# Optimization experiments

Measured on AMD Instinct MI355X. Metric: run time of the kernel, lower is better.

Reference implementation:

```python
import jax, jax.numpy as jnp
import numpy as np

N = 50000      # nodes
E = 800000     # edges (before self loops)
F_IN = 128     # dataset.num_features
HID = 32       # hidden_channels (per GAT head)
HEADS = 4
C = 40         # dataset.num_classes
NEG_SLOPE = 0.2


def setup_inputs() -> dict:
    key = jax.random.key(0)
    ks = jax.random.split(key, 18)
    g = lambda k, shape, fan: jax.random.normal(k, shape, dtype=jnp.float32) / np.sqrt(fan)
    inp = {
        "x": jax.random.normal(ks[0], (N, F_IN), dtype=jnp.float32),
        "edge_index": jax.random.randint(ks[1], (2, E), 0, N, dtype=jnp.int64),
        # GAT layer 1: F_IN -> HEADS*HID
        "gat_W1": g(ks[2], (F_IN, HEADS * HID), F_IN),
        "gat_att_src1": g(ks[3], (HEADS, HID), HID),
        "gat_att_dst1": g(ks[4], (HEADS, HID), HID),
        "gat_b1": jnp.zeros((HEADS * HID,), jnp.float32),
        # GAT layer 2: HEADS*HID -> C, heads=1
        "gat_W2": g(ks[5], (HEADS * HID, C), HEADS * HID),
        "gat_att_src2": g(ks[6], (1, C), C),
        "gat_att_dst2": g(ks[7], (1, C), C),
        "gat_b2": jnp.zeros((C,), jnp.float32),
        # GCN layers
        "gcn_W1": g(ks[8], (F_IN, HID), F_IN),
        "gcn_b1": jnp.zeros((HID,), jnp.float32),
        "gcn_W2": g(ks[9], (HID, C), HID),
        "gcn_b2": jnp.zeros((C,), jnp.float32),
        # final linear: 2C -> C
        "lin_W": g(ks[10], (2 * C, C), 2 * C),
        "lin_b": jnp.zeros((C,), jnp.float32),
        "weight_c": jnp.float32(0.5),
        "weight_t": jnp.float32(0.5),
    }
    return inp


def _add_self_loops(src, dst, n):
    loop = jnp.arange(n, dtype=src.dtype)
    return jnp.concatenate([src, loop]), jnp.concatenate([dst, loop])


def _gat_conv(x, src, dst, n, W, att_src, att_dst, b, heads, out_dim):
    # h: [n, heads, out_dim]
    h = (x @ W).reshape(n, heads, out_dim)
    a_s = jnp.einsum('nhd,hd->nh', h, att_src)   # source-side attention logit
    a_d = jnp.einsum('nhd,hd->nh', h, att_dst)   # target-side attention logit
    e = jax.nn.leaky_relu(a_s[src] + a_d[dst], NEG_SLOPE)  # [E', heads]
    # softmax over incoming edges of each target node (self loops guarantee >=1 edge)
    m = jax.ops.segment_max(e, dst, num_segments=n)
    ex = jnp.exp(e - m[dst])
    s = jax.ops.segment_sum(ex, dst, num_segments=n)
    alpha = ex / s[dst]                          # [E', heads]
    out = jax.ops.segment_sum(h[src] * alpha[..., None], dst, num_segments=n)
    return out.reshape(n, heads * out_dim) + b


def _gcn_conv(x, src, dst, n, W, b):
    h = x @ W
    deg = jax.ops.segment_sum(jnp.ones(src.shape, h.dtype), dst, num_segments=n)
    norm = jax.lax.rsqrt(deg)                    # deg >= 1 (self loops)
    coef = (norm[src] * norm[dst])[:, None]
    return jax.ops.segment_sum(h[src] * coef, dst, num_segments=n) + b


def reference(x, edge_index, gat_W1, gat_att_src1, gat_att_dst1, gat_b1,
              gat_W2, gat_att_src2, gat_att_dst2, gat_b2,
              gcn_W1, gcn_b1, gcn_W2, gcn_b2, lin_W, lin_b,
              weight_c, weight_t):
    n = x.shape[0]
    src, dst = _add_self_loops(edge_index[0], edge_index[1], n)
    # GAT branch (dropout is identity at inference)
    x_gat = _gat_conv(x, src, dst, n, gat_W1, gat_att_src1, gat_att_dst1,
                      gat_b1, HEADS, HID)
    x_gat = jax.nn.elu(x_gat)
    x_gat = _gat_conv(x_gat, src, dst, n, gat_W2, gat_att_src2, gat_att_dst2,
                      gat_b2, 1, C)
    # GCN branch
    x_gcn = jax.nn.relu(_gcn_conv(x, src, dst, n, gcn_W1, gcn_b1))
    x_gcn = _gcn_conv(x_gcn, src, dst, n, gcn_W2, gcn_b2)
    # weighted feature concat + linear head
    cat = jnp.concatenate([x_gcn * weight_c, x_gat * weight_t], axis=1)  # [n, 2C]
    return cat @ lin_W + lin_b
```

## Files before the change

### kernel.cpp

```cpp
#include <hip/hip_runtime.h>
#include <math.h>

#define F_IN   128
#define HIDC   32
#define NHEAD  4
#define CDIM   40
#define NEG_SLOPE 0.2f
#define BCAP   4096
#define OVCAP  16384
#define SCHUNK 4096

typedef __attribute__((ext_vector_type(8))) short bf16x8;
typedef __attribute__((ext_vector_type(4))) float f32x4;

__device__ __forceinline__ float leakyf(float x) { return x > 0.f ? x : NEG_SLOPE * x; }

__device__ __forceinline__ float wred_sum(float v) {
#pragma unroll
    for (int o = 32; o > 0; o >>= 1) v += __shfl_xor(v, o, 64);
    return v;
}
__device__ __forceinline__ float sel4(float4 v, int h) {
    return (h == 0) ? v.x : (h == 1) ? v.y : (h == 2) ? v.z : v.w;
}
__device__ __forceinline__ unsigned pack2_bf16(float a, float b) {
    unsigned ua = __float_as_uint(a);
    unsigned ub = __float_as_uint(b);
    ua = (ua + 0x7FFFu + ((ua >> 16) & 1u)) >> 16;
    ub = (ub + 0x7FFFu + ((ub >> 16) & 1u)) >> 16;
    return ua | (ub << 16);
}
__device__ __forceinline__ float2 unpack2_bf16(unsigned p) {
    return make_float2(__uint_as_float(p << 16), __uint_as_float(p & 0xFFFF0000u));
}
__device__ __forceinline__ float bf2f(unsigned short u) {
    return __uint_as_float(((unsigned)u) << 16);
}

__global__ void wb_prep_kernel(const float* __restrict__ Wg, const float* __restrict__ Wc,
                               uint4* __restrict__ wbf)
{
    int b = blockIdx.x;
    int lane = threadIdx.x;
    int nt = b >> 2, ks = b & 3;
    int c = nt * 16 + (lane & 15);
    int k0 = ks * 32 + (lane >> 4) * 8;
    unsigned u[4];
#pragma unroll
    for (int jj = 0; jj < 4; ++jj) {
        int k = k0 + 2 * jj;
        float a0 = (c < 128) ? Wg[(size_t)k * 128 + c] : Wc[(size_t)k * 32 + (c - 128)];
        float a1 = (c < 128) ? Wg[(size_t)(k + 1) * 128 + c] : Wc[(size_t)(k + 1) * 32 + (c - 128)];
        u[jj] = pack2_bf16(a0, a1);
    }
    wbf[(size_t)b * 64 + lane] = make_uint4(u[0], u[1], u[2], u[3]);
}

__global__ __launch_bounds__(256) void gemm1_mfma_kernel(
    const float* __restrict__ X, const uint4* __restrict__ wbf,
    const float* __restrict__ aw_s, const float* __restrict__ aw_d,
    unsigned* __restrict__ h1b, unsigned* __restrict__ g1b,
    float* __restrict__ as1, float* __restrict__ ad1, int n)
{
    __shared__ float Ct[64][164];
    __shared__ float sw[128], dw[128];
    const int tid = threadIdx.x;
    const int w = tid >> 6, lane = tid & 63;
    const int m = lane & 15, q = lane >> 4;
    const int node0 = blockIdx.x * 64;
    if (tid < 128) { sw[tid] = aw_s[tid]; dw[tid] = aw_d[tid]; }

    f32x4 acc[10];
#pragma unroll
    for (int t = 0; t < 10; ++t) acc[t] = (f32x4){0.f, 0.f, 0.f, 0.f};

    const int row = node0 + w * 16 + m;
    const bool rv = row < n;
#pragma unroll
    for (int ks = 0; ks < 4; ++ks) {
        uint4 pa = make_uint4(0u, 0u, 0u, 0u);
        if (rv) {
            const float* xr = X + (size_t)row * 128 + ks * 32 + q * 8;
            float4 a0 = *(const float4*)xr;
            float4 a1 = *(const float4*)(xr + 4);
            pa = make_uint4(pack2_bf16(a0.x, a0.y), pack2_bf16(a0.z, a0.w),
                            pack2_bf16(a1.x, a1.y), pack2_bf16(a1.z, a1.w));
        }
        bf16x8 af = *(bf16x8*)&pa;
#pragma unroll
        for (int nt = 0; nt < 10; ++nt) {
            uint4 pb = wbf[(size_t)(nt * 4 + ks) * 64 + lane];
            bf16x8 bfv = *(bf16x8*)&pb;
            acc[nt] = __builtin_amdgcn_mfma_f32_16x16x32_bf16(af, bfv, acc[nt], 0, 0, 0);
        }
    }
#pragma unroll
    for (int nt = 0; nt < 10; ++nt)
#pragma unroll
        for (int r = 0; r < 4; ++r)
            Ct[w * 16 + q * 4 + r][nt * 16 + m] = acc[nt][r];
    __syncthreads();

    for (int i = tid; i < 64 * 64; i += 256) {
        int nd = i >> 6, u = i & 63;
        int gn = node0 + nd;
        if (gn < n)
            h1b[(size_t)gn * 64 + u] = pack2_bf16(Ct[nd][2 * u], Ct[nd][2 * u + 1]);
    }
    for (int i = tid; i < 64 * 16; i += 256) {
        int nd = i >> 4, u = i & 15;
        int gn = node0 + nd;
        if (gn < n)
            g1b[(size_t)gn * 16 + u] = pack2_bf16(Ct[nd][128 + 2 * u], Ct[nd][128 + 2 * u + 1]);
    }
    {
        int nd = tid >> 2, h = tid & 3;
        int gn = node0 + nd;
        if (gn < n) {
            float s = 0.f, d = 0.f;
#pragma unroll
            for (int k = 0; k < HIDC; ++k) {
                float v = Ct[nd][h * HIDC + k];
                s = fmaf(v, sw[h * HIDC + k], s);
                d = fmaf(v, dw[h * HIDC + k], d);
            }
            as1[(size_t)gn * 4 + h] = s;
            ad1[(size_t)gn * 4 + h] = d;
        }
    }
}

template<int K, int OUTC, int BN, int BK, int OSTRIDE = OUTC>
__global__ __launch_bounds__((OUTC / 4) * (BN / 4)) void gemm_tile(
    const float* __restrict__ X, const float* __restrict__ W,
    const float* __restrict__ bias, float* __restrict__ Y, int n)
{
    constexpr int CG = OUTC / 4;
    constexpr int NG = BN / 4;
    constexpr int NT = CG * NG;
    __shared__ float Xs[BK][BN + 4];
    __shared__ float Ws[BK][OUTC];
    const int tid = threadIdx.x;
    const int cg = tid % CG, ng = tid / CG;
    const int node0 = blockIdx.x * BN;
    float acc[4][4] = {};

    for (int kb = 0; kb < K; kb += BK) {
        for (int idx = tid; idx < BN * (BK / 4); idx += NT) {
            int nd = idx / (BK / 4);
            int kq = idx % (BK / 4);
            int gnode = node0 + nd;
            float4 v = (gnode < n) ? *(const float4*)&X[(size_t)gnode * K + kb + kq * 4]
                                   : make_float4(0.f, 0.f, 0.f, 0.f);
            Xs[kq * 4 + 0][nd] = v.x;
            Xs[kq * 4 + 1][nd] = v.y;
            Xs[kq * 4 + 2][nd] = v.z;
            Xs[kq * 4 + 3][nd] = v.w;
        }
        for (int idx = tid; idx < BK * CG; idx += NT) {
            int kk = idx / CG;
            int cq = idx % CG;
            *(float4*)&Ws[kk][cq * 4] = *(const float4*)&W[(size_t)(kb + kk) * OUTC + cq * 4];
        }
        __syncthreads();
#pragma unroll
        for (int k = 0; k < BK; ++k) {
            float4 xv = *(const float4*)&Xs[k][ng * 4];
            float4 wv = *(const float4*)&Ws[k][cg * 4];
            float xa[4] = {xv.x, xv.y, xv.z, xv.w};
            float wa[4] = {wv.x, wv.y, wv.z, wv.w};
#pragma unroll
            for (int j = 0; j < 4; ++j)
#pragma unroll
                for (int c = 0; c < 4; ++c)
                    acc[j][c] = fmaf(xa[j], wa[c], acc[j][c]);
        }
        __syncthreads();
    }

    float4 bv = make_float4(0.f, 0.f, 0.f, 0.f);
    if (bias) bv = *(const float4*)&bias[cg * 4];
#pragma unroll
    for (int j = 0; j < 4; ++j) {
        int gnode = node0 + ng * 4 + j;
        if (gnode < n) {
            float4 o = make_float4(acc[j][0] + bv.x, acc[j][1] + bv.y,
                                   acc[j][2] + bv.z, acc[j][3] + bv.w);
            *(float4*)&Y[(size_t)gnode * OSTRIDE + cg * 4] = o;
        }
    }
}

template<int K, int OUTC, int BN, int BK, int OSTRIDE_U, int OFF_U>
__global__ __launch_bounds__((OUTC / 4) * (BN / 4)) void gemm_tile_bb(
    const unsigned* __restrict__ Xb, const float* __restrict__ W,
    unsigned* __restrict__ Yb, int n)
{
    constexpr int CG = OUTC / 4;
    constexpr int NG = BN / 4;
    constexpr int NT = CG * NG;
    __shared__ float Xs[BK][BN + 4];
    __shared__ float Ws[BK][OUTC];
    const int tid = threadIdx.x;
    const int cg = tid % CG, ng = tid / CG;
    const int node0 = blockIdx.x * BN;
    float acc[4][4] = {};

    for (int kb = 0; kb < K; kb += BK) {
        for (int idx = tid; idx < BN * (BK / 8); idx += NT) {
            int nd = idx / (BK / 8);
            int kq = idx % (BK / 8);
            int gnode = node0 + nd;
            uint4 v = (gnode < n) ? *(const uint4*)&Xb[(size_t)gnode * (K / 2) + kb / 2 + kq * 4]
                                  : make_uint4(0u, 0u, 0u, 0u);
            float2 a = unpack2_bf16(v.x), b = unpack2_bf16(v.y);
            float2 c = unpack2_bf16(v.z), d = unpack2_bf16(v.w);
            Xs[kq * 8 + 0][nd] = a.x; Xs[kq * 8 + 1][nd] = a.y;
            Xs[kq * 8 + 2][nd] = b.x; Xs[kq * 8 + 3][nd] = b.y;
            Xs[kq * 8 + 4][nd] = c.x; Xs[kq * 8 + 5][nd] = c.y;
            Xs[kq * 8 + 6][nd] = d.x; Xs[kq * 8 + 7][nd] = d.y;
        }
        for (int idx = tid; idx < BK * CG; idx += NT) {
            int kk = idx / CG;
            int cq = idx % CG;
            *(float4*)&Ws[kk][cq * 4] = *(const float4*)&W[(size_t)(kb + kk) * OUTC + cq * 4];
        }
        __syncthreads();
#pragma unroll
        for (int k = 0; k < BK; ++k) {
            float4 xv = *(const float4*)&Xs[k][ng * 4];
            float4 wv = *(const float4*)&Ws[k][cg * 4];
            float xa[4] = {xv.x, xv.y, xv.z, xv.w};
            float wa[4] = {wv.x, wv.y, wv.z, wv.w};
#pragma unroll
            for (int j = 0; j < 4; ++j)
#pragma unroll
                for (int c = 0; c < 4; ++c)
                    acc[j][c] = fmaf(xa[j], wa[c], acc[j][c]);
        }
        __syncthreads();
    }

#pragma unroll
    for (int j = 0; j < 4; ++j) {
        int gnode = node0 + ng * 4 + j;
        if (gnode < n) {
            uint2 pb = make_uint2(pack2_bf16(acc[j][0], acc[j][1]),
                                  pack2_bf16(acc[j][2], acc[j][3]));
            *(uint2*)&Yb[(size_t)gnode * OSTRIDE_U + OFF_U + cg * 2] = pb;
        }
    }
}

__global__ __launch_bounds__(320) void gemm2_gat_kernel(
    const unsigned* __restrict__ Xb, const float* __restrict__ W,
    const float* __restrict__ aw_s, const float* __restrict__ aw_d,
    unsigned* __restrict__ Yb, float* __restrict__ as2, float* __restrict__ ad2, int n)
{
    constexpr int K = 128, OUTC = 40, BN = 128, BK = 32;
    constexpr int CG = OUTC / 4, NT = 320;
    __shared__ float smem[32 * 132 + 32 * 40];
    float* Xs = smem;
    float* Ws = smem + 32 * 132;
    const int tid = threadIdx.x;
    const int cg = tid % CG, ng = tid / CG;
    const int node0 = blockIdx.x * BN;
    float acc[4][4] = {};

    for (int kb = 0; kb < K; kb += BK) {
        for (int idx = tid; idx < BN * (BK / 8); idx += NT) {
            int nd = idx / (BK / 8);
            int kq = idx % (BK / 8);
            int gnode = node0 + nd;
            uint4 v = (gnode < n) ? *(const uint4*)&Xb[(size_t)gnode * (K / 2) + kb / 2 + kq * 4]
                                  : make_uint4(0u, 0u, 0u, 0u);
            float2 a = unpack2_bf16(v.x), b = unpack2_bf16(v.y);
            float2 c = unpack2_bf16(v.z), d = unpack2_bf16(v.w);
            Xs[(kq * 8 + 0) * 132 + nd] = a.x; Xs[(kq * 8 + 1) * 132 + nd] = a.y;
            Xs[(kq * 8 + 2) * 132 + nd] = b.x; Xs[(kq * 8 + 3) * 132 + nd] = b.y;
            Xs[(kq * 8 + 4) * 132 + nd] = c.x; Xs[(kq * 8 + 5) * 132 + nd] = c.y;
            Xs[(kq * 8 + 6) * 132 + nd] = d.x; Xs[(kq * 8 + 7) * 132 + nd] = d.y;
        }
        for (int idx = tid; idx < BK * CG; idx += NT) {
            int kk = idx / CG;
            int cq = idx % CG;
            *(float4*)&Ws[kk * 40 + cq * 4] = *(const float4*)&W[(size_t)(kb + kk) * OUTC + cq * 4];
        }
        __syncthreads();
#pragma unroll
        for (int k = 0; k < BK; ++k) {
            float4 xv = *(const float4*)&Xs[k * 132 + ng * 4];
            float4 wv = *(const float4*)&Ws[k * 40 + cg * 4];
            float xa[4] = {xv.x, xv.y, xv.z, xv.w};
            float wa[4] = {wv.x, wv.y, wv.z, wv.w};
#pragma unroll
            for (int j = 0; j < 4; ++j)
#pragma unroll
                for (int c = 0; c < 4; ++c)
                    acc[j][c] = fmaf(xa[j], wa[c], acc[j][c]);
        }
        __syncthreads();
    }

    float* Ct  = smem;
    float* sww = smem + 128 * 41;
    float* dww = sww + 40;
#pragma unroll
    for (int j = 0; j < 4; ++j) {
        int gnode = node0 + ng * 4 + j;
        if (gnode < n) {
            uint2 pb = make_uint2(pack2_bf16(acc[j][0], acc[j][1]),
                                  pack2_bf16(acc[j][2], acc[j][3]));
            *(uint2*)&Yb[(size_t)gnode * 40 + cg * 2] = pb;
        }
#pragma unroll
        for (int c = 0; c < 4; ++c)
            Ct[(ng * 4 + j) * 41 + cg * 4 + c] = acc[j][c];
    }
    if (tid < 40) { sww[tid] = aw_s[tid]; dww[tid] = aw_d[tid]; }
    __syncthreads();
    if (tid < 128) {
        int gnode = node0 + tid;
        if (gnode < n) {
            float s = 0.f, d = 0.f;
#pragma unroll
            for (int c = 0; c < 40; ++c) {
                float v = Ct[tid * 41 + c];
                s = fmaf(v, sww[c], s);
                d = fmaf(v, dww[c], d);
            }
            as2[gnode] = s;
            ad2[gnode] = d;
        }
    }
}

__global__ __launch_bounds__(256) void bucket_scatter_kernel(
    const int* __restrict__ src, const int* __restrict__ dst,
    unsigned* __restrict__ bcnt, unsigned* __restrict__ bpair,
    unsigned* __restrict__ ovf_cnt, uint2* __restrict__ ovf, int e, int nbuck)
{
    __shared__ unsigned hist[512];
    __shared__ unsigned base[512];
    const int t = threadIdx.x;
    const int lo = blockIdx.x * SCHUNK;
    const int hi = min(lo + SCHUNK, e);
    for (int i = t; i < nbuck; i += 256) hist[i] = 0;
    __syncthreads();
    for (int i = lo + t; i < hi; i += 256)
        atomicAdd(&hist[((unsigned)dst[i]) >> 7], 1u);
    __syncthreads();
    for (int i = t; i < nbuck; i += 256) {
        unsigned c = hist[i];
        base[i] = c ? atomicAdd(&bcnt[i], c) : 0u;
        hist[i] = 0;
    }
    __syncthreads();
    for (int i = lo + t; i < hi; i += 256) {
        unsigned s = (unsigned)src[i], d = (unsigned)dst[i];
        unsigned b = d >> 7;
        unsigned pos = base[b] + atomicAdd(&hist[b], 1u);
        if (pos < BCAP) bpair[(size_t)b * BCAP + pos] = s | ((d & 127u) << 16);
        else {
            unsigned o = atomicAdd(ovf_cnt, 1u);
            if (o < OVCAP) ovf[o] = make_uint2(s, d);
        }
    }
}

__global__ __launch_bounds__(256) void bucket_count_kernel(
    const unsigned* __restrict__ bcnt, const unsigned* __restrict__ bpair,
    const unsigned* __restrict__ ovf_cnt, const uint2* __restrict__ ovf,
    unsigned* __restrict__ counts, int n)
{
    __shared__ unsigned lc[128];
    const int b = blockIdx.x, base = b << 7;
    if (threadIdx.x < 128) lc[threadIdx.x] = 0;
    __syncthreads();
    unsigned bc = bcnt[b];
    int cnt = (int)(bc < BCAP ? bc : BCAP);
    for (int k = threadIdx.x; k < cnt; k += 256)
        atomicAdd(&lc[bpair[(size_t)b * BCAP + k] >> 16], 1u);
    unsigned oc_u = *ovf_cnt;
    int oc = (int)(oc_u < OVCAP ? oc_u : OVCAP);
    for (int k = threadIdx.x; k < oc; k += 256) {
        uint2 pp = ovf[k];
        if ((int)(pp.y >> 7) == b) atomicAdd(&lc[pp.y & 127u], 1u);
    }
    __syncthreads();
    int i = base + threadIdx.x;
    if (threadIdx.x < 128 && i < n) counts[i] = lc[threadIdx.x];
}

__global__ __launch_bounds__(256) void scan_reduce_kernel(const unsigned* __restrict__ counts,
                                                          unsigned* __restrict__ partials, int n)
{
    __shared__ unsigned sm[256];
    int t = threadIdx.x;
    int i = blockIdx.x * 256 + t;
    unsigned v = (i < n) ? counts[i] : 0u;
    sm[t] = v;
    __syncthreads();
#pragma unroll
    for (int off = 128; off > 0; off >>= 1) {
        if (t < off) sm[t] += sm[t + off];
        __syncthreads();
    }
    if (t == 0) partials[blockIdx.x] = sm[0];
}

__global__ __launch_bounds__(256) void scan_partials_kernel(unsigned* __restrict__ partials,
                                                            unsigned* __restrict__ rs, int nb, int n)
{
    __shared__ unsigned sm[256];
    int t = threadIdx.x;
    unsigned v = (t < nb) ? partials[t] : 0u;
    sm[t] = v;
    __syncthreads();
#pragma unroll
    for (int off = 1; off < 256; off <<= 1) {
        unsigned u = (t >= off) ? sm[t - off] : 0u;
        __syncthreads();
        sm[t] += u;
        __syncthreads();
    }
    if (t < nb) partials[t] = sm[t] - v;
    if (t == 255) rs[n] = sm[255];
}

__global__ __launch_bounds__(256) void scan_write_kernel(const unsigned* __restrict__ counts,
                                                         const unsigned* __restrict__ partials,
                                                         unsigned* __restrict__ rs,
                                                         float* __restrict__ nrm, int n)
{
    __shared__ unsigned sm[256];
    int t = threadIdx.x;
    int i = blockIdx.x * 256 + t;
    unsigned c = (i < n) ? counts[i] : 0u;
    sm[t] = c;
    __syncthreads();
#pragma unroll
    for (int off = 1; off < 256; off <<= 1) {
        unsigned u = (t >= off) ? sm[t - off] : 0u;
        __syncthreads();
        sm[t] += u;
        __syncthreads();
    }
    if (i < n) {
        rs[i] = partials[blockIdx.x] + sm[t] - c;
        nrm[i] = rsqrtf((float)(c + 1u));
    }
}

__global__ __launch_bounds__(256) void bucket_place_kernel(
    const unsigned* __restrict__ bcnt, const unsigned* __restrict__ bpair,
    const unsigned* __restrict__ rs, unsigned* __restrict__ csr_src,
    unsigned* __restrict__ cursor, int n)
{
    __shared__ unsigned lc[128];
    __shared__ unsigned rbase[128];
    const int b = blockIdx.x, base = b << 7;
    if (threadIdx.x < 128) {
        lc[threadIdx.x] = 0;
        int i = base + threadIdx.x;
        rbase[threadIdx.x] = (i < n) ? rs[i] : 0u;
    }
    __syncthreads();
    unsigned bc = bcnt[b];
    int cnt = (int)(bc < BCAP ? bc : BCAP);
    for (int k = threadIdx.x; k < cnt; k += 256) {
        unsigned v = bpair[(size_t)b * BCAP + k];
        unsigned ld = v >> 16;
        unsigned r = atomicAdd(&lc[ld], 1u);
        csr_src[rbase[ld] + r] = v & 0xFFFFu;
    }
    __syncthreads();
    int i = base + threadIdx.x;
    if (threadIdx.x < 128 && i < n) cursor[i] = rbase[threadIdx.x] + lc[threadIdx.x];
}

__global__ void overflow_fill_kernel(const unsigned* __restrict__ ovf_cnt,
                                     const uint2* __restrict__ ovf,
                                     unsigned* __restrict__ cursor,
                                     unsigned* __restrict__ csr_src)
{
    unsigned oc_u = *ovf_cnt;
    int oc = (int)(oc_u < OVCAP ? oc_u : OVCAP);
    for (int k = threadIdx.x; k < oc; k += 256) {
        uint2 pp = ovf[k];
        unsigned pos = atomicAdd(&cursor[pp.y], 1u);
        csr_src[pos] = pp.x;
    }
}

#define CAP1 96
__global__ __launch_bounds__(256) void agg1_fused_kernel(
    const unsigned* __restrict__ h1b, const unsigned short* __restrict__ g1b,
    const float* __restrict__ as1, const float* __restrict__ ad1,
    const float* __restrict__ nrm,
    const unsigned* __restrict__ rs, const unsigned* __restrict__ csr_src,
    const float* __restrict__ gat_b1, const float* __restrict__ gcn_b1,
    unsigned* __restrict__ xgb, unsigned* __restrict__ gaccb, int n)
{
    __shared__ unsigned sidx[4][CAP1];
    __shared__ float    w4[4][CAP1][4];
    __shared__ float    cf[4][CAP1];
    const int wid = threadIdx.x >> 6;
    const int lane = threadIdx.x & 63;
    const int i = blockIdx.x * 4 + wid;
    if (i >= n) return;
    const unsigned beg = rs[i];
    const int deg = (int)(rs[i + 1] - beg);
    const float4* as1v = (const float4*)as1;
    float4 av = as1v[i];
    float4 dv = ((const float4*)ad1)[i];
    const float ni = nrm[i];
    float4 ese = make_float4(__expf(leakyf(av.x + dv.x)), __expf(leakyf(av.y + dv.y)),
                             __expf(leakyf(av.z + dv.z)), __expf(leakyf(av.w + dv.w)));
    float s0 = 0.f, s1 = 0.f, s2 = 0.f, s3 = 0.f;
    for (int k = lane; k < deg; k += 64) {
        unsigned s = csr_src[beg + k];
        float4 a = as1v[s];
        float w0 = __expf(leakyf(a.x + dv.x)), w1 = __expf(leakyf(a.y + dv.y));
        float w2 = __expf(leakyf(a.z + dv.z)), w3 = __expf(leakyf(a.w + dv.w));
        if (k < CAP1) {
            sidx[wid][k] = s;
            w4[wid][k][0] = w0; w4[wid][k][1] = w1;
            w4[wid][k][2] = w2; w4[wid][k][3] = w3;
            cf[wid][k] = nrm[s];
        }
        s0 += w0; s1 += w1; s2 += w2; s3 += w3;
    }
    if (lane == 0) { s0 += ese.x; s1 += ese.y; s2 += ese.z; s3 += ese.w; }
    s0 = wred_sum(s0); s1 = wred_sum(s1); s2 = wred_sum(s2); s3 = wred_sum(s3);
    __threadfence_block();
    const int h = lane >> 4;
    const float advh = sel4(dv, h);
    const float ssh  = sel4(make_float4(s0, s1, s2, s3), h);
    const float wself = sel4(ese, h);
    const bool gact = lane < 32;
    float2 hv = unpack2_bf16(h1b[(size_t)i * 64 + lane]);
    float2 acc = make_float2(hv.x * wself, hv.y * wself);
    float gacc = gact ? bf2f(g1b[(size_t)i * 32 + lane]) * ni * ni : 0.f;
    const int dcB = deg < CAP1 ? deg : CAP1;
    int j = 0;
    for (; j + 4 <= dcB; j += 4) {
        unsigned ss[4]; float ww[4], cc[4];
#pragma unroll
        for (int t = 0; t < 4; ++t) {
            ss[t] = sidx[wid][j + t];
            ww[t] = w4[wid][j + t][h];
            cc[t] = cf[wid][j + t];
        }
        unsigned pv[4];
#pragma unroll
        for (int t = 0; t < 4; ++t) pv[t] = h1b[(size_t)ss[t] * 64 + lane];
        float gv[4];
        if (gact) {
#pragma unroll
            for (int t = 0; t < 4; ++t) gv[t] = bf2f(g1b[(size_t)ss[t] * 32 + lane]);
        }
#pragma unroll
        for (int t = 0; t < 4; ++t) {
            float2 v = unpack2_bf16(pv[t]);
            acc.x = fmaf(v.x, ww[t], acc.x);
            acc.y = fmaf(v.y, ww[t], acc.y);
            if (gact) gacc = fmaf(gv[t], cc[t] * ni, gacc);
        }
    }
    for (; j < dcB; ++j) {
        unsigned s = sidx[wid][j];
        float w = w4[wid][j][h], c = cf[wid][j];
        float2 v = unpack2_bf16(h1b[(size_t)s * 64 + lane]);
        acc.x = fmaf(v.x, w, acc.x);
        acc.y = fmaf(v.y, w, acc.y);
        if (gact) gacc = fmaf(bf2f(g1b[(size_t)s * 32 + lane]), c * ni, gacc);
    }
    for (; j < deg; ++j) {
        unsigned s = csr_src[beg + j];
        float4 a = as1v[s];
        float w = __expf(leakyf(sel4(a, h) + advh));
        float c = nrm[s];
        float2 v = unpack2_bf16(h1b[(size_t)s * 64 + lane]);
        acc.x = fmaf(v.x, w, acc.x);
        acc.y = fmaf(v.y, w, acc.y);
        if (gact) gacc = fmaf(bf2f(g1b[(size_t)s * 32 + lane]), c * ni, gacc);
    }
    float inv = 1.f / ssh;
    int c0 = 2 * lane;
    float o0 = acc.x * inv + gat_b1[c0];
    float o1 = acc.y * inv + gat_b1[c0 + 1];
    o0 = o0 > 0.f ? o0 : __expf(o0) - 1.f;
    o1 = o1 > 0.f ? o1 : __expf(o1) - 1.f;
    xgb[(size_t)i * 64 + lane] = pack2_bf16(o0, o1);
    float go = gact ? fmaxf(gacc + gcn_b1[lane], 0.f) : 0.f;
    float gp = __shfl_xor(go, 1, 64);
    if (gact && (lane & 1) == 0)
        gaccb[(size_t)i * 16 + (lane >> 1)] = pack2_bf16(go, gp);
}

#define CAP2 128
__global__ __launch_bounds__(256) void agg2_fused_kernel(
    const unsigned* __restrict__ hg_b, const float* __restrict__ as2,
    const float* __restrict__ ad2, const float* __restrict__ nrm,
    const unsigned* __restrict__ rs, const unsigned* __restrict__ csr_src,
    const float* __restrict__ gat_b2, const float* __restrict__ gcn_b2,
    const float* __restrict__ wc_p, const float* __restrict__ wt_p,
    float* __restrict__ cat, int n)
{
    __shared__ unsigned sidx[4][CAP2];
    __shared__ float    wgt[4][CAP2];
    __shared__ float    cf [4][CAP2];
    const int wid = threadIdx.x >> 6;
    const int lane = threadIdx.x & 63;
    const int i = blockIdx.x * 4 + wid;
    if (i >= n) return;
    const unsigned beg = rs[i];
    const int deg = (int)(rs[i + 1] - beg);
    const float adv = ad2[i];
    const float eself = __expf(leakyf(as2[i] + adv));
    const float ni = nrm[i];
    float ssum = (lane == 0) ? eself : 0.f;
    for (int k = lane; k < deg; k += 64) {
        unsigned s = csr_src[beg + k];
        float w = __expf(leakyf(as2[s] + adv));
        if (k < CAP2) { sidx[wid][k] = s; wgt[wid][k] = w; cf[wid][k] = nrm[s]; }
        ssum += w;
    }
    ssum = wred_sum(ssum);
    __threadfence_block();
    const bool act   = lane < 40;
    const bool isgat = lane < 20;
    const float selfw = isgat ? eself : ni * ni;
    float2 acc = make_float2(0.f, 0.f);
    if (act) {
        float2 v = unpack2_bf16(hg_b[(size_t)i * 40 + lane]);
        acc.x = v.x * selfw; acc.y = v.y * selfw;
    }
    const int dcB = deg < CAP2 ? deg : CAP2;
    int j = 0;
    for (; j + 4 <= dcB; j += 4) {
        unsigned ss[4]; float ww[4];
#pragma unroll
        for (int t = 0; t < 4; ++t) {
            ss[t] = sidx[wid][j + t];
            ww[t] = isgat ? wgt[wid][j + t] : cf[wid][j + t] * ni;
        }
        if (act) {
#pragma unroll
            for (int t = 0; t < 4; ++t) {
                float2 v = unpack2_bf16(hg_b[(size_t)ss[t] * 40 + lane]);
                acc.x = fmaf(v.x, ww[t], acc.x);
                acc.y = fmaf(v.y, ww[t], acc.y);
            }
        }
    }
    for (; j < dcB; ++j) {
        unsigned s = sidx[wid][j];
        float w = isgat ? wgt[wid][j] : cf[wid][j] * ni;
        if (act) {
            float2 v = unpack2_bf16(hg_b[(size_t)s * 40 + lane]);
            acc.x = fmaf(v.x, w, acc.x); acc.y = fmaf(v.y, w, acc.y);
        }
    }
    for (; j < deg; ++j) {
        unsigned s = csr_src[beg + j];
        float w = isgat ? __expf(leakyf(as2[s] + adv)) : nrm[s] * ni;
        if (act) {
            float2 v = unpack2_bf16(hg_b[(size_t)s * 40 + lane]);
            acc.x = fmaf(v.x, w, acc.x); acc.y = fmaf(v.y, w, acc.y);
        }
    }
    if (act) {
        if (isgat) {
            float inv = 1.f / ssum, wt = *wt_p;
            int c0 = 2 * lane;
            cat[(size_t)i * 80 + 40 + c0]     = (acc.x * inv + gat_b2[c0]) * wt;
            cat[(size_t)i * 80 + 40 + c0 + 1] = (acc.y * inv + gat_b2[c0 + 1]) * wt;
        } else {
            float wc = *wc_p;
            int c0 = 2 * (lane - 20);
            cat[(size_t)i * 80 + c0]     = (acc.x + gcn_b2[c0]) * wc;
            cat[(size_t)i * 80 + c0 + 1] = (acc.y + gcn_b2[c0 + 1]) * wc;
        }
    }
}

extern "C" void kernel_launch(void* const* d_in, const int* in_sizes, int n_in,
                              void* d_out, int out_size, void* d_ws, size_t ws_size,
                              hipStream_t stream)
{
    const float* x        = (const float*)d_in[0];
    const int*   eidx     = (const int*)d_in[1];
    const float* gat_W1   = (const float*)d_in[2];
    const float* att_s1   = (const float*)d_in[3];
    const float* att_d1   = (const float*)d_in[4];
    const float* gat_b1   = (const float*)d_in[5];
    const float* gat_W2   = (const float*)d_in[6];
    const float* att_s2   = (const float*)d_in[7];
    const float* att_d2   = (const float*)d_in[8];
    const float* gat_b2   = (const float*)d_in[9];
    const float* gcn_W1   = (const float*)d_in[10];
    const float* gcn_b1   = (const float*)d_in[11];
    const float* gcn_W2   = (const float*)d_in[12];
    const float* gcn_b2   = (const float*)d_in[13];
    const float* lin_W    = (const float*)d_in[14];
    const float* lin_b    = (const float*)d_in[15];
    const float* wc_p     = (const float*)d_in[16];
    const float* wt_p     = (const float*)d_in[17];

    const int n = in_sizes[0] / F_IN;
    const int e = in_sizes[1] / 2;
    const int* src = eidx;
    const int* dst = eidx + e;
    const int NBUCK = (n + 127) >> 7;

    char* p = (char*)d_ws;
    auto alloc = [&](size_t bytes) -> void* {
        void* r = (void*)p;
        p += (bytes + 255) & ~(size_t)255;
        return r;
    };
    unsigned* counts  = (unsigned*)alloc((size_t)n * 4);
    unsigned* rs      = (unsigned*)alloc((size_t)(n + 1) * 4);
    unsigned* cursor  = (unsigned*)alloc((size_t)n * 4);
    unsigned* partials= (unsigned*)alloc(256 * 4);
    unsigned* bcnt    = (unsigned*)alloc((size_t)(NBUCK + 1) * 4);
    unsigned* csr_src = (unsigned*)alloc((size_t)e * 4);
    uint4*    wbf     = (uint4*)alloc(40 * 64 * 16);
    float* nrm     = (float*)alloc((size_t)n * 4);
    float* as1     = (float*)alloc((size_t)n * 4 * 4);
    float* ad1     = (float*)alloc((size_t)n * 4 * 4);
    float* as2     = (float*)alloc((size_t)n * 4);
    float* ad2     = (float*)alloc((size_t)n * 4);
    float* cat     = (float*)alloc((size_t)n * 80 * 4);
    unsigned* hg_b = (unsigned*)alloc((size_t)n * 40 * 4);
    float* xg      = (float*)alloc((size_t)n * F_IN * 4);
    unsigned* g1b  = (unsigned*)alloc((size_t)n * 16 * 4);
    unsigned* gaccb= (unsigned*)alloc((size_t)n * 16 * 4);
    unsigned* bpair = (unsigned*)cat;
    uint2*    ovf   = (uint2*)(bpair + (size_t)NBUCK * BCAP);
    unsigned* h1b   = (unsigned*)cat;
    unsigned* xgb   = (unsigned*)xg;
    unsigned* ovf_cnt = bcnt + NBUCK;

    const int NB = (n + 255) / 256;
    const int WB = (n + 3) / 4;
    const int SB = (e + SCHUNK - 1) / SCHUNK;

    hipMemsetAsync(bcnt, 0, (size_t)(NBUCK + 1) * 4, stream);
    bucket_scatter_kernel<<<SB, 256, 0, stream>>>(src, dst, bcnt, bpair, ovf_cnt, ovf, e, NBUCK);
    bucket_count_kernel<<<NBUCK, 256, 0, stream>>>(bcnt, bpair, ovf_cnt, ovf, counts, n);
    scan_reduce_kernel<<<NB, 256, 0, stream>>>(counts, partials, n);
    scan_partials_kernel<<<1, 256, 0, stream>>>(partials, rs, NB, n);
    scan_write_kernel<<<NB, 256, 0, stream>>>(counts, partials, rs, nrm, n);
    bucket_place_kernel<<<NBUCK, 256, 0, stream>>>(bcnt, bpair, rs, csr_src, cursor, n);
    overflow_fill_kernel<<<1, 256, 0, stream>>>(ovf_cnt, ovf, cursor, csr_src);

    wb_prep_kernel<<<40, 64, 0, stream>>>(gat_W1, gcn_W1, wbf);
    gemm1_mfma_kernel<<<(n + 63) / 64, 256, 0, stream>>>(x, wbf, att_s1, att_d1,
                                                         h1b, g1b, as1, ad1, n);

    agg1_fused_kernel<<<WB, 256, 0, stream>>>(h1b, (const unsigned short*)g1b,
                                              as1, ad1, nrm, rs, csr_src,
                                              gat_b1, gcn_b1, xgb, gaccb, n);

    gemm_tile_bb<32, 40, 128, 32, 40, 20><<<(n + 127) / 128, 320, 0, stream>>>(gaccb, gcn_W2, hg_b, n);
    gemm2_gat_kernel<<<(n + 127) / 128, 320, 0, stream>>>(xgb, gat_W2, att_s2, att_d2,
                                                          hg_b, as2, ad2, n);

    agg2_fused_kernel<<<WB, 256, 0, stream>>>(hg_b, as2, ad2, nrm, rs, csr_src,
                                              gat_b2, gcn_b2, wc_p, wt_p, cat, n);

    gemm_tile<80, 40, 128, 40><<<(n + 127) / 128, 320, 0, stream>>>(cat, lin_W, lin_b, (float*)d_out, n);
}
```

Baseline: 306.9 us.

## Vectorize neighbor gathers in aggregation kernels with 16-byte loads across edge groups

Both fused aggregation kernels now split each wavefront so several lanes each handle a different edge and read 16-byte uint4 chunks (8 bf16 features) of a neighbor row, instead of one 4-byte word per lane per edge. Partial sums are combined with cross-lane shuffles at the end, and the cached neighbor lists are padded to a multiple of four with zero-weight self entries. The GCN normalization product is precomputed in shared memory. The aim is fewer, wider memory transactions and more edges in flight per wave. In exchange it adds shuffle reductions and more registers per lane, and the overflow path beyond the cache capacity runs on only a subset of lanes.

```diff
diff --git a/kernel.cpp b/kernel.cpp
--- a/kernel.cpp
+++ b/kernel.cpp
@@ -495,7 +495,7 @@
 
 #define CAP1 96
 __global__ __launch_bounds__(256) void agg1_fused_kernel(
-    const unsigned* __restrict__ h1b, const unsigned short* __restrict__ g1b,
+    const unsigned* __restrict__ h1b, const unsigned* __restrict__ g1b,
     const float* __restrict__ as1, const float* __restrict__ ad1,
     const float* __restrict__ nrm,
     const unsigned* __restrict__ rs, const unsigned* __restrict__ csr_src,
@@ -504,7 +504,7 @@
 {
     __shared__ unsigned sidx[4][CAP1];
     __shared__ float    w4[4][CAP1][4];
-    __shared__ float    cf[4][CAP1];
+    __shared__ float    cfs[4][CAP1];
     const int wid = threadIdx.x >> 6;
     const int lane = threadIdx.x & 63;
     const int i = blockIdx.x * 4 + wid;
@@ -525,78 +525,135 @@
         float w2 = __expf(leakyf(a.z + dv.z)), w3 = __expf(leakyf(a.w + dv.w));
         if (k < CAP1) {
             sidx[wid][k] = s;
-            w4[wid][k][0] = w0; w4[wid][k][1] = w1;
-            w4[wid][k][2] = w2; w4[wid][k][3] = w3;
-            cf[wid][k] = nrm[s];
+            *(float4*)&w4[wid][k][0] = make_float4(w0, w1, w2, w3);
+            cfs[wid][k] = nrm[s] * ni;
         }
         s0 += w0; s1 += w1; s2 += w2; s3 += w3;
+    }
+    const int dc  = deg < CAP1 ? deg : CAP1;
+    const int dc4 = (dc + 3) & ~3;
+    if (lane < dc4 - dc) {
+        int k = dc + lane;
+        sidx[wid][k] = (unsigned)i;
+        *(float4*)&w4[wid][k][0] = make_float4(0.f, 0.f, 0.f, 0.f);
+        cfs[wid][k] = 0.f;
     }
     if (lane == 0) { s0 += ese.x; s1 += ese.y; s2 += ese.z; s3 += ese.w; }
     s0 = wred_sum(s0); s1 = wred_sum(s1); s2 = wred_sum(s2); s3 = wred_sum(s3);
     __threadfence_block();
-    const int h = lane >> 4;
-    const float advh = sel4(dv, h);
-    const float ssh  = sel4(make_float4(s0, s1, s2, s3), h);
-    const float wself = sel4(ese, h);
-    const bool gact = lane < 32;
-    float2 hv = unpack2_bf16(h1b[(size_t)i * 64 + lane]);
-    float2 acc = make_float2(hv.x * wself, hv.y * wself);
-    float gacc = gact ? bf2f(g1b[(size_t)i * 32 + lane]) * ni * ni : 0.f;
-    const int dcB = deg < CAP1 ? deg : CAP1;
-    int j = 0;
-    for (; j + 4 <= dcB; j += 4) {
-        unsigned ss[4]; float ww[4], cc[4];
-#pragma unroll
-        for (int t = 0; t < 4; ++t) {
-            ss[t] = sidx[wid][j + t];
-            ww[t] = w4[wid][j + t][h];
-            cc[t] = cf[wid][j + t];
-        }
-        unsigned pv[4];
-#pragma unroll
-        for (int t = 0; t < 4; ++t) pv[t] = h1b[(size_t)ss[t] * 64 + lane];
-        float gv[4];
+
+    const int e = lane >> 4, c = lane & 15;
+    const int h = c >> 2;
+    const float ssh = sel4(make_float4(s0, s1, s2, s3), h);
+    const int e2 = lane >> 2, c2 = lane & 3;
+    const bool gact = lane < 16;
+    const uint4* h1v = (const uint4*)h1b;
+    const uint4* g1v = (const uint4*)g1b;
+
+    float acc[8], gacc[8];
+#pragma unroll
+    for (int t = 0; t < 8; ++t) { acc[t] = 0.f; gacc[t] = 0.f; }
+
+    if (e == 0) {
+        uint4 hv = h1v[(size_t)i * 16 + c];
+        float wself = sel4(ese, h);
+        float2 p0 = unpack2_bf16(hv.x), p1 = unpack2_bf16(hv.y);
+        float2 p2 = unpack2_bf16(hv.z), p3 = unpack2_bf16(hv.w);
+        acc[0] = p0.x * wself; acc[1] = p0.y * wself;
+        acc[2] = p1.x * wself; acc[3] = p1.y * wself;
+        acc[4] = p2.x * wself; acc[5] = p2.y * wself;
+        acc[6] = p3.x * wself; acc[7] = p3.y * wself;
+    }
+    if (lane < 4) {
+        uint4 gv = g1v[(size_t)i * 4 + lane];
+        float w2s = ni * ni;
+        float2 q0 = unpack2_bf16(gv.x), q1 = unpack2_bf16(gv.y);
+        float2 q2 = unpack2_bf16(gv.z), q3 = unpack2_bf16(gv.w);
+        gacc[0] = q0.x * w2s; gacc[1] = q0.y * w2s;
+        gacc[2] = q1.x * w2s; gacc[3] = q1.y * w2s;
+        gacc[4] = q2.x * w2s; gacc[5] = q2.y * w2s;
+        gacc[6] = q3.x * w2s; gacc[7] = q3.y * w2s;
+    }
+
+    for (int j = 0; j < dc4; j += 4) {
+        unsigned s = sidx[wid][j + e];
+        float    w = w4[wid][j + e][h];
+        uint4 hv = h1v[(size_t)s * 16 + c];
+        float2 p0 = unpack2_bf16(hv.x), p1 = unpack2_bf16(hv.y);
+        float2 p2 = unpack2_bf16(hv.z), p3 = unpack2_bf16(hv.w);
+        acc[0] = fmaf(p0.x, w, acc[0]); acc[1] = fmaf(p0.y, w, acc[1]);
+        acc[2] = fmaf(p1.x, w, acc[2]); acc[3] = fmaf(p1.y, w, acc[3]);
+        acc[4] = fmaf(p2.x, w, acc[4]); acc[5] = fmaf(p2.y, w, acc[5]);
+        acc[6] = fmaf(p3.x, w, acc[6]); acc[7] = fmaf(p3.y, w, acc[7]);
         if (gact) {
-#pragma unroll
-            for (int t = 0; t < 4; ++t) gv[t] = bf2f(g1b[(size_t)ss[t] * 32 + lane]);
-        }
-#pragma unroll
-        for (int t = 0; t < 4; ++t) {
-            float2 v = unpack2_bf16(pv[t]);
-            acc.x = fmaf(v.x, ww[t], acc.x);
-            acc.y = fmaf(v.y, ww[t], acc.y);
-            if (gact) gacc = fmaf(gv[t], cc[t] * ni, gacc);
-        }
-    }
-    for (; j < dcB; ++j) {
-        unsigned s = sidx[wid][j];
-        float w = w4[wid][j][h], c = cf[wid][j];
-        float2 v = unpack2_bf16(h1b[(size_t)s * 64 + lane]);
-        acc.x = fmaf(v.x, w, acc.x);
-        acc.y = fmaf(v.y, w, acc.y);
-        if (gact) gacc = fmaf(bf2f(g1b[(size_t)s * 32 + lane]), c * ni, gacc);
-    }
-    for (; j < deg; ++j) {
+            unsigned s2 = sidx[wid][j + e2];
+            float    cw = cfs[wid][j + e2];
+            uint4 gv = g1v[(size_t)s2 * 4 + c2];
+            float2 q0 = unpack2_bf16(gv.x), q1 = unpack2_bf16(gv.y);
+            float2 q2 = unpack2_bf16(gv.z), q3 = unpack2_bf16(gv.w);
+            gacc[0] = fmaf(q0.x, cw, gacc[0]); gacc[1] = fmaf(q0.y, cw, gacc[1]);
+            gacc[2] = fmaf(q1.x, cw, gacc[2]); gacc[3] = fmaf(q1.y, cw, gacc[3]);
+            gacc[4] = fmaf(q2.x, cw, gacc[4]); gacc[5] = fmaf(q2.y, cw, gacc[5]);
+            gacc[6] = fmaf(q3.x, cw, gacc[6]); gacc[7] = fmaf(q3.y, cw, gacc[7]);
+        }
+    }
+    for (int j = CAP1; j < deg; ++j) {
         unsigned s = csr_src[beg + j];
-        float4 a = as1v[s];
-        float w = __expf(leakyf(sel4(a, h) + advh));
-        float c = nrm[s];
-        float2 v = unpack2_bf16(h1b[(size_t)s * 64 + lane]);
-        acc.x = fmaf(v.x, w, acc.x);
-        acc.y = fmaf(v.y, w, acc.y);
-        if (gact) gacc = fmaf(bf2f(g1b[(size_t)s * 32 + lane]), c * ni, gacc);
-    }
-    float inv = 1.f / ssh;
-    int c0 = 2 * lane;
-    float o0 = acc.x * inv + gat_b1[c0];
-    float o1 = acc.y * inv + gat_b1[c0 + 1];
-    o0 = o0 > 0.f ? o0 : __expf(o0) - 1.f;
-    o1 = o1 > 0.f ? o1 : __expf(o1) - 1.f;
-    xgb[(size_t)i * 64 + lane] = pack2_bf16(o0, o1);
-    float go = gact ? fmaxf(gacc + gcn_b1[lane], 0.f) : 0.f;
-    float gp = __shfl_xor(go, 1, 64);
-    if (gact && (lane & 1) == 0)
-        gaccb[(size_t)i * 16 + (lane >> 1)] = pack2_bf16(go, gp);
+        if (e == 0) {
+            float4 a = as1v[s];
+            float w = __expf(leakyf(sel4(a, h) + sel4(dv, h)));
+            uint4 hv = h1v[(size_t)s * 16 + c];
+            float2 p0 = unpack2_bf16(hv.x), p1 = unpack2_bf16(hv.y);
+            float2 p2 = unpack2_bf16(hv.z), p3 = unpack2_bf16(hv.w);
+            acc[0] = fmaf(p0.x, w, acc[0]); acc[1] = fmaf(p0.y, w, acc[1]);
+            acc[2] = fmaf(p1.x, w, acc[2]); acc[3] = fmaf(p1.y, w, acc[3]);
+            acc[4] = fmaf(p2.x, w, acc[4]); acc[5] = fmaf(p2.y, w, acc[5]);
+            acc[6] = fmaf(p3.x, w, acc[6]); acc[7] = fmaf(p3.y, w, acc[7]);
+        }
+        if (lane < 4) {
+            float cw = nrm[s] * ni;
+            uint4 gv = g1v[(size_t)s * 4 + lane];
+            float2 q0 = unpack2_bf16(gv.x), q1 = unpack2_bf16(gv.y);
+            float2 q2 = unpack2_bf16(gv.z), q3 = unpack2_bf16(gv.w);
+            gacc[0] = fmaf(q0.x, cw, gacc[0]); gacc[1] = fmaf(q0.y, cw, gacc[1]);
+            gacc[2] = fmaf(q1.x, cw, gacc[2]); gacc[3] = fmaf(q1.y, cw, gacc[3]);
+            gacc[4] = fmaf(q2.x, cw, gacc[4]); gacc[5] = fmaf(q2.y, cw, gacc[5]);
+            gacc[6] = fmaf(q3.x, cw, gacc[6]); gacc[7] = fmaf(q3.y, cw, gacc[7]);
+        }
+    }
+
+#pragma unroll
+    for (int t = 0; t < 8; ++t) {
+        acc[t]  += __shfl_xor(acc[t], 16, 64);
+        acc[t]  += __shfl_xor(acc[t], 32, 64);
+        gacc[t] += __shfl_xor(gacc[t], 4, 64);
+        gacc[t] += __shfl_xor(gacc[t], 8, 64);
+    }
+    if (e == 0) {
+        float inv = 1.f / ssh;
+        float4 b0 = *(const float4*)&gat_b1[c * 8];
+        float4 b1 = *(const float4*)&gat_b1[c * 8 + 4];
+        float o[8] = {acc[0] * inv + b0.x, acc[1] * inv + b0.y,
+                      acc[2] * inv + b0.z, acc[3] * inv + b0.w,
+                      acc[4] * inv + b1.x, acc[5] * inv + b1.y,
+                      acc[6] * inv + b1.z, acc[7] * inv + b1.w};
+#pragma unroll
+        for (int t = 0; t < 8; ++t) o[t] = o[t] > 0.f ? o[t] : __expf(o[t]) - 1.f;
+        uint4 pv = make_uint4(pack2_bf16(o[0], o[1]), pack2_bf16(o[2], o[3]),
+                              pack2_bf16(o[4], o[5]), pack2_bf16(o[6], o[7]));
+        ((uint4*)xgb)[(size_t)i * 16 + c] = pv;
+    }
+    if (lane < 4) {
+        float4 b0 = *(const float4*)&gcn_b1[lane * 8];
+        float4 b1 = *(const float4*)&gcn_b1[lane * 8 + 4];
+        float g[8] = {fmaxf(gacc[0] + b0.x, 0.f), fmaxf(gacc[1] + b0.y, 0.f),
+                      fmaxf(gacc[2] + b0.z, 0.f), fmaxf(gacc[3] + b0.w, 0.f),
+                      fmaxf(gacc[4] + b1.x, 0.f), fmaxf(gacc[5] + b1.y, 0.f),
+                      fmaxf(gacc[6] + b1.z, 0.f), fmaxf(gacc[7] + b1.w, 0.f)};
+        uint4 pv = make_uint4(pack2_bf16(g[0], g[1]), pack2_bf16(g[2], g[3]),
+                              pack2_bf16(g[4], g[5]), pack2_bf16(g[6], g[7]));
+        ((uint4*)gaccb)[(size_t)i * 4 + lane] = pv;
+    }
 }
 
 #define CAP2 128
@@ -610,7 +667,7 @@
 {
     __shared__ unsigned sidx[4][CAP2];
     __shared__ float    wgt[4][CAP2];
-    __shared__ float    cf [4][CAP2];
+    __shared__ float    cfn[4][CAP2];
     const int wid = threadIdx.x >> 6;
     const int lane = threadIdx.x & 63;
     const int i = blockIdx.x * 4 + wid;
@@ -624,64 +681,90 @@
     for (int k = lane; k < deg; k += 64) {
         unsigned s = csr_src[beg + k];
         float w = __expf(leakyf(as2[s] + adv));
-        if (k < CAP2) { sidx[wid][k] = s; wgt[wid][k] = w; cf[wid][k] = nrm[s]; }
+        if (k < CAP2) { sidx[wid][k] = s; wgt[wid][k] = w; cfn[wid][k] = nrm[s] * ni; }
         ssum += w;
+    }
+    const int dc  = deg < CAP2 ? deg : CAP2;
+    const int dc4 = (dc + 3) & ~3;
+    if (lane < dc4 - dc) {
+        int k = dc + lane;
+        sidx[wid][k] = (unsigned)i; wgt[wid][k] = 0.f; cfn[wid][k] = 0.f;
     }
     ssum = wred_sum(ssum);
     __threadfence_block();
-    const bool act   = lane < 40;
-    const bool isgat = lane < 20;
-    const float selfw = isgat ? eself : ni * ni;
-    float2 acc = make_float2(0.f, 0.f);
+
+    const int e = lane & 3, c = lane >> 2;
+    const bool act = c < 10;
+    const bool isgat = c < 5;
+    const float* wptr = isgat ? &wgt[wid][0] : &cfn[wid][0];
+    const uint4* hgv = (const uint4*)hg_b;
+
+    float acc[8];
+#pragma unroll
+    for (int t = 0; t < 8; ++t) acc[t] = 0.f;
+    if (act && e == 0) {
+        uint4 hv = hgv[(size_t)i * 10 + c];
+        float sw = isgat ? eself : ni * ni;
+        float2 p0 = unpack2_bf16(hv.x), p1 = unpack2_bf16(hv.y);
+        float2 p2 = unpack2_bf16(hv.z), p3 = unpack2_bf16(hv.w);
+        acc[0] = p0.x * sw; acc[1] = p0.y * sw;
+        acc[2] = p1.x * sw; acc[3] = p1.y * sw;
+        acc[4] = p2.x * sw; acc[5] = p2.y * sw;
+        acc[6] = p3.x * sw; acc[7] = p3.y * sw;
+    }
     if (act) {
-        float2 v = unpack2_bf16(hg_b[(size_t)i * 40 + lane]);
-        acc.x = v.x * selfw; acc.y = v.y * selfw;
-    }
-    const int dcB = deg < CAP2 ? deg : CAP2;
-    int j = 0;
-    for (; j + 4 <= dcB; j += 4) {
-        unsigned ss[4]; float ww[4];
-#pragma unroll
-        for (int t = 0; t < 4; ++t) {
-            ss[t] = sidx[wid][j + t];
-            ww[t] = isgat ? wgt[wid][j + t] : cf[wid][j + t] * ni;
-        }
-        if (act) {
-#pragma unroll
-            for (int t = 0; t < 4; ++t) {
-                float2 v = unpack2_bf16(hg_b[(size_t)ss[t] * 40 + lane]);
-                acc.x = fmaf(v.x, ww[t], acc.x);
-                acc.y = fmaf(v.y, ww[t], acc.y);
+        for (int j = 0; j < dc4; j += 4) {
+            unsigned s = sidx[wid][j + e];
+            float    w = wptr[j + e];
+            uint4 hv = hgv[(size_t)s * 10 + c];
+            float2 p0 = unpack2_bf16(hv.x), p1 = unpack2_bf16(hv.y);
+            float2 p2 = unpack2_bf16(hv.z), p3 = unpack2_bf16(hv.w);
+            acc[0] = fmaf(p0.x, w, acc[0]); acc[1] = fmaf(p0.y, w, acc[1]);
+            acc[2] = fmaf(p1.x, w, acc[2]); acc[3] = fmaf(p1.y, w, acc[3]);
+            acc[4] = fmaf(p2.x, w, acc[4]); acc[5] = fmaf(p2.y, w, acc[5]);
+            acc[6] = fmaf(p3.x, w, acc[6]); acc[7] = fmaf(p3.y, w, acc[7]);
+        }
+        for (int j = CAP2; j < deg; ++j) {
+            if (e == 0) {
+                unsigned s = csr_src[beg + j];
+                float w = isgat ? __expf(leakyf(as2[s] + adv)) : nrm[s] * ni;
+                uint4 hv = hgv[(size_t)s * 10 + c];
+                float2 p0 = unpack2_bf16(hv.x), p1 = unpack2_bf16(hv.y);
+                float2 p2 = unpack2_bf16(hv.z), p3 = unpack2_bf16(hv.w);
+                acc[0] = fmaf(p0.x, w, acc[0]); acc[1] = fmaf(p0.y, w, acc[1]);
+                acc[2] = fmaf(p1.x, w, acc[2]); acc[3] = fmaf(p1.y, w, acc[3]);
+                acc[4] = fmaf(p2.x, w, acc[4]); acc[5] = fmaf(p2.y, w, acc[5]);
+                acc[6] = fmaf(p3.x, w, acc[6]); acc[7] = fmaf(p3.y, w, acc[7]);
             }
         }
     }
-    for (; j < dcB; ++j) {
-        unsigned s = sidx[wid][j];
-        float w = isgat ? wgt[wid][j] : cf[wid][j] * ni;
-        if (act) {
-            float2 v = unpack2_bf16(hg_b[(size_t)s * 40 + lane]);
-            acc.x = fmaf(v.x, w, acc.x); acc.y = fmaf(v.y, w, acc.y);
-        }
-    }
-    for (; j < deg; ++j) {
-        unsigned s = csr_src[beg + j];
-        float w = isgat ? __expf(leakyf(as2[s] + adv)) : nrm[s] * ni;
-        if (act) {
-            float2 v = unpack2_bf16(hg_b[(size_t)s * 40 + lane]);
-            acc.x = fmaf(v.x, w, acc.x); acc.y = fmaf(v.y, w, acc.y);
-        }
-    }
-    if (act) {
+#pragma unroll
+    for (int t = 0; t < 8; ++t) {
+        acc[t] += __shfl_xor(acc[t], 1, 64);
+        acc[t] += __shfl_xor(acc[t], 2, 64);
+    }
+    if (act && e == 0) {
         if (isgat) {
             float inv = 1.f / ssum, wt = *wt_p;
-            int c0 = 2 * lane;
-            cat[(size_t)i * 80 + 40 + c0]     = (acc.x * inv + gat_b2[c0]) * wt;
-            cat[(size_t)i * 80 + 40 + c0 + 1] = (acc.y * inv + gat_b2[c0 + 1]) * wt;
+            float4 b0 = *(const float4*)&gat_b2[c * 8];
+            float4 b1 = *(const float4*)&gat_b2[c * 8 + 4];
+            float4 o0 = make_float4((acc[0] * inv + b0.x) * wt, (acc[1] * inv + b0.y) * wt,
+                                    (acc[2] * inv + b0.z) * wt, (acc[3] * inv + b0.w) * wt);
+            float4 o1 = make_float4((acc[4] * inv + b1.x) * wt, (acc[5] * inv + b1.y) * wt,
+                                    (acc[6] * inv + b1.z) * wt, (acc[7] * inv + b1.w) * wt);
+            *(float4*)&cat[(size_t)i * 80 + 40 + c * 8]     = o0;
+            *(float4*)&cat[(size_t)i * 80 + 40 + c * 8 + 4] = o1;
         } else {
             float wc = *wc_p;
-            int c0 = 2 * (lane - 20);
-            cat[(size_t)i * 80 + c0]     = (acc.x + gcn_b2[c0]) * wc;
-            cat[(size_t)i * 80 + c0 + 1] = (acc.y + gcn_b2[c0 + 1]) * wc;
+            int g = c - 5;
+            float4 b0 = *(const float4*)&gcn_b2[g * 8];
+            float4 b1 = *(const float4*)&gcn_b2[g * 8 + 4];
+            float4 o0 = make_float4((acc[0] + b0.x) * wc, (acc[1] + b0.y) * wc,
+                                    (acc[2] + b0.z) * wc, (acc[3] + b0.w) * wc);
+            float4 o1 = make_float4((acc[4] + b1.x) * wc, (acc[5] + b1.y) * wc,
+                                    (acc[6] + b1.z) * wc, (acc[7] + b1.w) * wc);
+            *(float4*)&cat[(size_t)i * 80 + g * 8]     = o0;
+            *(float4*)&cat[(size_t)i * 80 + g * 8 + 4] = o1;
         }
     }
 }
@@ -761,8 +844,7 @@
     gemm1_mfma_kernel<<<(n + 63) / 64, 256, 0, stream>>>(x, wbf, att_s1, att_d1,
                                                          h1b, g1b, as1, ad1, n);
 
-    agg1_fused_kernel<<<WB, 256, 0, stream>>>(h1b, (const unsigned short*)g1b,
-                                              as1, ad1, nrm, rs, csr_src,
+    agg1_fused_kernel<<<WB, 256, 0, stream>>>(h1b, g1b, as1, ad1, nrm, rs, csr_src,
                                               gat_b1, gcn_b1, xgb, gaccb, n);
 
     gemm_tile_bb<32, 40, 128, 32, 40, 20><<<(n + 127) / 128, 320, 0, stream>>>(gaccb, gcn_W2, hg_b, n);
```

After: 309.8 us. Within noise of the previous version (+0.9%).
